# Performance work log

Measured on AMD Instinct MI355X. Metric: run time of the kernel, lower is better.

## Reference

```python
import jax, jax.numpy as jnp
import numpy as np

N = 100000   # nodes
E = 1600000  # edges
D_IN = 128
D_H = 128


def setup_inputs() -> dict:
    key = jax.random.key(0)
    ks = jax.random.split(key, 8)
    s = 1.0 / np.sqrt(D_IN)
    return {
        "x": jax.random.normal(ks[0], (N, D_IN), dtype=jnp.float32),
        "edge_index": jax.random.randint(ks[1], (2, E), 0, N, dtype=jnp.int64),
        "W_l1": jax.random.uniform(ks[2], (D_IN, D_H), jnp.float32, -s, s),
        "b_l1": jnp.zeros((D_H,), jnp.float32),
        "W_r1": jax.random.uniform(ks[3], (D_IN, D_H), jnp.float32, -s, s),
        "W_l2": jax.random.uniform(ks[4], (D_H, D_H), jnp.float32, -s, s),
        "b_l2": jnp.zeros((D_H,), jnp.float32),
        "W_r2": jax.random.uniform(ks[5], (D_H, D_H), jnp.float32, -s, s),
    }


def _sage_layer(z, src, dst, Wl, bl, Wr):
    # message: relu(x_j) gathered along src; aggregate: mean over dst
    msg = jax.nn.relu(z[src])                                   # [E, D]
    summed = jax.ops.segment_sum(msg, dst, num_segments=N)      # [N, D]
    cnt = jax.ops.segment_sum(jnp.ones((src.shape[0],), z.dtype), dst,
                              num_segments=N)                   # [N]
    mean = summed / jnp.maximum(cnt, 1.0)[:, None]
    return mean @ Wl + bl + z @ Wr                              # lin_l + lin_r(root)


def reference(x, edge_index, W_l1, b_l1, W_r1, W_l2, b_l2, W_r2):
    src, dst = edge_index[0], edge_index[1]
    h = _sage_layer(x, src, dst, W_l1, b_l1, W_r1)
    h = jax.nn.relu(h)  # activation between layers; norms are Identity, dropout 0
    return _sage_layer(h, src, dst, W_l2, b_l2, W_r2)
```

## Files before the change

kernel.cpp:

```cpp
#include <hip/hip_runtime.h>

typedef short short8 __attribute__((ext_vector_type(8)));
typedef unsigned short ushort8 __attribute__((ext_vector_type(8)));
typedef float f32x4 __attribute__((ext_vector_type(4)));
typedef float f32x2 __attribute__((ext_vector_type(2)));

__device__ __forceinline__ unsigned short f2bf(float f) {
    unsigned int u = __float_as_uint(f);
    u += 0x7FFFu + ((u >> 16) & 1u);
    return (unsigned short)(u >> 16);
}
__device__ __forceinline__ float bf2f(unsigned short s) {
    return __uint_as_float(((unsigned int)s) << 16);
}


#define BSHIFT 8
#define BCAP   8192
#define EPB    2048
#define STG    4792

__global__ __launch_bounds__(512) void prep_k(const int* __restrict__ ei,
                                              int* __restrict__ bcnt,
                                              unsigned int* __restrict__ bbuf,
                                              int E, int B,
                                              const float* __restrict__ x,
                                              unsigned int* __restrict__ xq,
                                              unsigned int* __restrict__ hqz,
                                              int total4,
                                              const float* __restrict__ W0,
                                              const float* __restrict__ W1,
                                              const float* __restrict__ W2,
                                              const float* __restrict__ W3,
                                              unsigned short* __restrict__ wsz,
                                              int P1B, int CXB) {
    __shared__ int s_cnt[512];
    __shared__ int s_off[512];
    __shared__ int s_wsum[8];
    __shared__ int s_wbase[8];
    __shared__ unsigned int s_gmap[608];
    __shared__ unsigned int stage[STG];
    __shared__ int s_T;
    int tid = threadIdx.x;
    int bx = blockIdx.x;

    if (bx < P1B) {
        s_cnt[tid] = 0;
        __syncthreads();
        int e0 = bx * EPB + tid;
        int dstc[4];
#pragma unroll
        for (int k = 0; k < 4; k++) {
            int e = e0 + k * 512;
            dstc[k] = (e < E) ? ei[E + e] : -1;
            if (e < E) atomicAdd(&s_cnt[dstc[k] >> BSHIFT], 1);
        }
        __syncthreads();
        int c = s_cnt[tid];
        int cpad = (c + 7) & ~7;
        int lane = tid & 63, wid = tid >> 6;
        int incl = cpad;
#pragma unroll
        for (int d = 1; d < 64; d <<= 1) {
            int t = __shfl_up(incl, d);
            if (lane >= d) incl += t;
        }
        if (lane == 63) s_wsum[wid] = incl;
        __syncthreads();
        if (tid < 8) {
            int acc = 0;
            for (int j = 0; j < tid; j++) acc += s_wsum[j];
            s_wbase[tid] = acc;
            if (tid == 7) s_T = acc + s_wsum[7];
        }
        __syncthreads();
        int excl = s_wbase[wid] + incl - cpad;
        int gbase = (c > 0) ? atomicAdd(&bcnt[tid], cpad) : 0;
        unsigned int bb = (unsigned int)tid * BCAP;
        int ng = cpad >> 3;
        for (int k = 0; k < ng; k++) {
            int gw = gbase + (k << 3);
            s_gmap[(excl >> 3) + k] = (gw + 8 <= BCAP) ? (bb + (unsigned int)gw) : 0xFFFFFFFFu;
        }
        for (int j = c; j < cpad; j++) stage[excl + j] = 0xFFFFFFFFu;
        s_off[tid] = excl;
        s_cnt[tid] = 0;
        __syncthreads();
#pragma unroll
        for (int k = 0; k < 4; k++) {
            int e = e0 + k * 512;
            if (e < E) {
                int src = ei[e];
                int dst = dstc[k];
                int b = dst >> BSHIFT;
                int pos = s_off[b] + atomicAdd(&s_cnt[b], 1);
                stage[pos] = ((unsigned int)(dst & 255) << 17) | (unsigned int)src;
            }
        }
        __syncthreads();
        int T = s_T;
        for (int i = tid; i < T; i += 512) {
            unsigned int g = s_gmap[i >> 3];
            if (g != 0xFFFFFFFFu) bbuf[(size_t)g + (i & 7)] = stage[i];
        }
    } else if (bx < P1B + CXB) {
        int base = (bx - P1B) * 2048 + tid;
#pragma unroll
        for (int k = 0; k < 4; k++) {
            int i = base + k * 512;
            if (i < total4) {
                float4 v = ((const float4*)x)[i];
                float rx = fmaxf(v.x, 0.f), ry = fmaxf(v.y, 0.f);
                float rz = fmaxf(v.z, 0.f), rw = fmaxf(v.w, 0.f);
                unsigned int q = (unsigned int)__builtin_amdgcn_cvt_pk_fp8_f32(rx, ry, 0, false);
                q = (unsigned int)__builtin_amdgcn_cvt_pk_fp8_f32(rz, rw, (int)q, true);
                xq[i] = q;
            } else if (i < total4 + 32) {
                xq[i] = 0;
                hqz[i - total4] = 0;
            }
        }
    } else {
        int idx = (bx - P1B - CXB) * 512 + tid;
        if (idx < 4 * 16384) {
            int m = idx >> 14, r = idx & 16383;
            const float* W = (m == 0) ? W0 : (m == 1) ? W1 : (m == 2) ? W2 : W3;
            int k = r >> 7, n = r & 127;
            int t = k >> 5, kg = (k >> 3) & 3, j = k & 7;
            int c = n >> 4, ln = n & 15;
            int dst = (((t * 8 + c) * 64) + kg * 16 + ln) * 8 + j;
            wsz[m * 16384 + dst] = f2bf(W[r]);
        }
    }
}

__global__ __launch_bounds__(512) void p2_k(const unsigned int* __restrict__ bbuf,
                                            const int* __restrict__ bcnt,
                                            int* __restrict__ col,
                                            int* __restrict__ deg, int N) {
    __shared__ int s_deg[256];
    int tid = threadIdx.x;
    int b = blockIdx.x;
    if (tid < 256) s_deg[tid] = 0;
    __syncthreads();
    int cnt = bcnt[b];
    if (cnt > BCAP) cnt = BCAP;
    int nbase = b << BSHIFT;
    for (int i = tid; i < cnt; i += 512) {
        unsigned int p = bbuf[(size_t)b * BCAP + i];
        if (p == 0xFFFFFFFFu) continue;
        int src = (int)(p & 0x1FFFFu);
        int rem = (int)(p >> 17);
        int slot = atomicAdd(&s_deg[rem], 1);
        if (slot < 64) col[(size_t)(nbase + rem) * 64 + slot] = src;
    }
    __syncthreads();
    int n = nbase + tid;
    if (tid < 256 && n < N) {
        int d = s_deg[tid];
        deg[n] = d;
        int dc = min(d, 64);
        int pe = min((dc + 3) & ~3, 64);
        for (int j = dc; j < pe; j++) col[(size_t)n * 64 + j] = N;
    }
}


__global__ __launch_bounds__(256) void agg_q(const unsigned char* __restrict__ hq,
                                             const int* __restrict__ col,
                                             const int* __restrict__ deg,
                                             unsigned short* __restrict__ mean,
                                             int N) {
    int lane = threadIdx.x & 63;
    int g = lane >> 4, l16 = lane & 15;
    int n = (blockIdx.x * 4 + (threadIdx.x >> 6)) * 4 + g;
    if (n >= N) return;
    int m = deg[n];
    if (m > 64) m = 64;
    const int* cp = col + (size_t)n * 64;
    unsigned int lofs = (unsigned int)l16 * 8u;

    f32x2 a[4];
#pragma unroll
    for (int d = 0; d < 4; d++) { a[d].x = 0.f; a[d].y = 0.f; }

    int s0 = cp[0], s1 = cp[1], s2 = cp[2], s3 = cp[3];

#pragma unroll 2
    for (int i = 0; i < m; i += 4) {
        uint2 v0 = *(const uint2*)(hq + ((((unsigned int)s0) << 7) + lofs));
        uint2 v1 = *(const uint2*)(hq + ((((unsigned int)s1) << 7) + lofs));
        uint2 v2 = *(const uint2*)(hq + ((((unsigned int)s2) << 7) + lofs));
        uint2 v3 = *(const uint2*)(hq + ((((unsigned int)s3) << 7) + lofs));
        s0 = cp[i + 4]; s1 = cp[i + 5]; s2 = cp[i + 6]; s3 = cp[i + 7];
#pragma unroll
        for (int k = 0; k < 4; k++) {
            uint2 v = (k == 0) ? v0 : (k == 1) ? v1 : (k == 2) ? v2 : v3;
            f32x2 p0 = __builtin_amdgcn_cvt_pk_f32_fp8((int)v.x, false);
            f32x2 p1 = __builtin_amdgcn_cvt_pk_f32_fp8((int)v.x, true);
            f32x2 p2 = __builtin_amdgcn_cvt_pk_f32_fp8((int)v.y, false);
            f32x2 p3 = __builtin_amdgcn_cvt_pk_f32_fp8((int)v.y, true);
            asm("v_pk_add_f32 %0, %0, %1" : "+v"(a[0]) : "v"(p0));
            asm("v_pk_add_f32 %0, %0, %1" : "+v"(a[1]) : "v"(p1));
            asm("v_pk_add_f32 %0, %0, %1" : "+v"(a[2]) : "v"(p2));
            asm("v_pk_add_f32 %0, %0, %1" : "+v"(a[3]) : "v"(p3));
        }
    }

    float iv = 1.0f / (float)max(m, 1);
    ushort8 p;
#pragma unroll
    for (int d = 0; d < 4; d++) {
        p[2 * d]     = f2bf(a[d].x * iv);
        p[2 * d + 1] = f2bf(a[d].y * iv);
    }
    *(ushort8*)((char*)mean + ((((unsigned int)n) << 8) + (unsigned int)l16 * 16u)) = p;
}


template <bool RELU, bool ZF32, bool OUT_BF16, bool OUT_Q>
__global__ __launch_bounds__(256) void gemm_fused(const unsigned short* __restrict__ A,
                                                  const void* __restrict__ Zv,
                                                  const unsigned short* __restrict__ wsz,
                                                  const float* __restrict__ bias,
                                                  float* __restrict__ outF,
                                                  unsigned short* __restrict__ outB,
                                                  unsigned char* __restrict__ outQ,
                                                  int M, int NG) {
    __shared__ unsigned short smem[32768];
    {
        const int4* src = (const int4*)wsz;
        int4* dst = (int4*)smem;
        for (int i = threadIdx.x; i < 4096; i += 256) dst[i] = src[i];
    }
    __syncthreads();

    int lane = threadIdx.x & 63;
    int wv = threadIdx.x >> 6;
    int r16 = lane & 15, kg = lane >> 4;

    for (int gq = blockIdx.x * 4 + wv; gq < NG; gq += gridDim.x * 4) {
        int rbase = gq * 64;
        short8 af[4][4], zf[4][4];
#pragma unroll
        for (int i = 0; i < 4; i++) {
            int row = rbase + i * 16 + r16;
            if (row < M) {
                const short8* ap = (const short8*)(A + (size_t)row * 128);
#pragma unroll
                for (int t = 0; t < 4; t++) af[i][t] = ap[t * 4 + kg];
                if (ZF32) {
                    const float4* zp = (const float4*)((const float*)Zv + (size_t)row * 128);
#pragma unroll
                    for (int t = 0; t < 4; t++) {
                        float4 a0 = zp[t * 8 + kg * 2];
                        float4 a1 = zp[t * 8 + kg * 2 + 1];
                        short8 z;
                        z[0] = (short)f2bf(a0.x); z[1] = (short)f2bf(a0.y);
                        z[2] = (short)f2bf(a0.z); z[3] = (short)f2bf(a0.w);
                        z[4] = (short)f2bf(a1.x); z[5] = (short)f2bf(a1.y);
                        z[6] = (short)f2bf(a1.z); z[7] = (short)f2bf(a1.w);
                        zf[i][t] = z;
                    }
                } else {
                    const short8* zp = (const short8*)((const unsigned short*)Zv + (size_t)row * 128);
#pragma unroll
                    for (int t = 0; t < 4; t++) zf[i][t] = zp[t * 4 + kg];
                }
            } else {
                short8 zr = {0, 0, 0, 0, 0, 0, 0, 0};
#pragma unroll
                for (int t = 0; t < 4; t++) { af[i][t] = zr; zf[i][t] = zr; }
            }
        }
#pragma unroll
        for (int c = 0; c < 8; c++) {
            float bv = bias[c * 16 + r16];
            f32x4 acc[4];
#pragma unroll
            for (int i = 0; i < 4; i++) acc[i] = (f32x4){bv, bv, bv, bv};
#pragma unroll
            for (int t = 0; t < 4; t++) {
                short8 wa = *(const short8*)(smem + ((t * 8 + c) * 64 + lane) * 8);
#pragma unroll
                for (int i = 0; i < 4; i++)
                    acc[i] = __builtin_amdgcn_mfma_f32_16x16x32_bf16(af[i][t], wa, acc[i], 0, 0, 0);
            }
#pragma unroll
            for (int t = 0; t < 4; t++) {
                short8 wb = *(const short8*)(smem + 16384 + ((t * 8 + c) * 64 + lane) * 8);
#pragma unroll
                for (int i = 0; i < 4; i++)
                    acc[i] = __builtin_amdgcn_mfma_f32_16x16x32_bf16(zf[i][t], wb, acc[i], 0, 0, 0);
            }
#pragma unroll
            for (int i = 0; i < 4; i++) {
#pragma unroll
                for (int r = 0; r < 4; r++) {
                    int orow = rbase + i * 16 + kg * 4 + r;
                    if (orow < M) {
                        float v = acc[i][r];
                        if (RELU) v = fmaxf(v, 0.f);
                        if (OUT_BF16)
                            outB[(size_t)orow * 128 + c * 16 + r16] = f2bf(v);
                        else
                            outF[(size_t)orow * 128 + c * 16 + r16] = v;
                        if (OUT_Q) {
                            unsigned int q = (unsigned int)__builtin_amdgcn_cvt_pk_fp8_f32(v, v, 0, false);
                            outQ[(size_t)orow * 128 + c * 16 + r16] = (unsigned char)(q & 0xFFu);
                        }
                    }
                }
            }
        }
    }
}


extern "C" void kernel_launch(void* const* d_in, const int* in_sizes, int n_in,
                              void* d_out, int out_size, void* d_ws, size_t ws_size,
                              hipStream_t stream) {
    const float* x   = (const float*)d_in[0];
    const int*   ei  = (const int*)d_in[1];
    const float* Wl1 = (const float*)d_in[2];
    const float* bl1 = (const float*)d_in[3];
    const float* Wr1 = (const float*)d_in[4];
    const float* Wl2 = (const float*)d_in[5];
    const float* bl2 = (const float*)d_in[6];
    const float* Wr2 = (const float*)d_in[7];

    int N = in_sizes[0] / 128;
    int E = in_sizes[1] / 2;
    int B = (N + 255) >> BSHIFT;

    char* ws = (char*)d_ws;
    size_t off = 0;
    auto alloc = [&](size_t bytes) -> char* {
        char* p = ws + off;
        off += (bytes + 255) & ~(size_t)255;
        return p;
    };
    int*   deg  = (int*)alloc((size_t)N * 4);
    int*   bcnt = (int*)alloc((size_t)B * 4);
    unsigned short* meanB = (unsigned short*)alloc((size_t)N * 128 * 2);
    unsigned short* hb    = (unsigned short*)alloc((size_t)(N + 1) * 128 * 2);
    unsigned short* wsz   = (unsigned short*)alloc(4 * 16384 * 2);

    unsigned int* bbuf = (unsigned int*)meanB;
    unsigned char* xq  = (unsigned char*)hb;
    int* col = (int*)d_out;
    unsigned char* hq = (unsigned char*)d_out + (size_t)N * 64 * 4;

    hipMemsetAsync(bcnt, 0, (size_t)B * 4, stream);

    int total4 = N * 32;
    int P1B = (E + EPB - 1) / EPB;
    int CXB = (total4 + 32 + 2047) / 2048;
    int CWB = (4 * 16384 + 511) / 512;
    prep_k<<<P1B + CXB + CWB, 512, 0, stream>>>(
        ei, bcnt, bbuf, E, B,
        x, (unsigned int*)xq, (unsigned int*)(hq + (size_t)N * 128), total4,
        Wl1, Wr1, Wl2, Wr2, wsz, P1B, CXB);
    p2_k<<<B, 512, 0, stream>>>(bbuf, bcnt, col, deg, N);

    int NT = (N + 15) / 16;
    int NG = (NT + 3) / 4;
    int GB = (NG + 3) / 4;
    agg_q<<<(N + 15) / 16, 256, 0, stream>>>(xq, col, deg, meanB, N);
    gemm_fused<true, true, true, true><<<GB, 256, 0, stream>>>(meanB, x, wsz, bl1,
                                                               nullptr, hb, hq, N, NG);
    agg_q<<<(N + 15) / 16, 256, 0, stream>>>(hq, col, deg, meanB, N);
    gemm_fused<false, false, false, false><<<GB, 256, 0, stream>>>(meanB, hb, wsz + 32768, bl2,
                                                                   (float*)d_out, nullptr, nullptr, N, NG);
}
```

Before: 271.8 us.

## Fuse neighbor mean aggregation into the MFMA GEMM kernels

Removes the separate agg_q kernels and performs the fp8 neighbor gather and mean inside each GEMM wave, building the bf16 A fragments directly in registers. This drops the bf16 mean buffer's write and read-back and two kernel launches. Workspace is reorganized: the col list moves out of d_out, the hidden bf16 layer is stored in d_out with a 512-byte row stride, and the second layer overwrites it in place. In exchange, each row's gather is spread over only 4 lanes with strided 8-byte loads, register pressure rises, and the GEMM grid is small. The gather may therefore become latency-bound with little parallelism to hide it.

```diff
diff --git a/kernel.cpp b/kernel.cpp
--- a/kernel.cpp
+++ b/kernel.cpp
@@ -10,8 +10,16 @@
     u += 0x7FFFu + ((u >> 16) & 1u);
     return (unsigned short)(u >> 16);
 }
-__device__ __forceinline__ float bf2f(unsigned short s) {
-    return __uint_as_float(((unsigned int)s) << 16);
+
+__device__ __forceinline__ void acc8(f32x2* a, uint2 v) {
+    f32x2 p0 = __builtin_amdgcn_cvt_pk_f32_fp8((int)v.x, false);
+    f32x2 p1 = __builtin_amdgcn_cvt_pk_f32_fp8((int)v.x, true);
+    f32x2 p2 = __builtin_amdgcn_cvt_pk_f32_fp8((int)v.y, false);
+    f32x2 p3 = __builtin_amdgcn_cvt_pk_f32_fp8((int)v.y, true);
+    asm("v_pk_add_f32 %0, %0, %1" : "+v"(a[0]) : "v"(p0));
+    asm("v_pk_add_f32 %0, %0, %1" : "+v"(a[1]) : "v"(p1));
+    asm("v_pk_add_f32 %0, %0, %1" : "+v"(a[2]) : "v"(p2));
+    asm("v_pk_add_f32 %0, %0, %1" : "+v"(a[3]) : "v"(p3));
 }
 
 
@@ -26,7 +34,6 @@
                                               int E, int B,
                                               const float* __restrict__ x,
                                               unsigned int* __restrict__ xq,
-                                              unsigned int* __restrict__ hqz,
                                               int total4,
                                               const float* __restrict__ W0,
                                               const float* __restrict__ W1,
@@ -117,7 +124,6 @@
                 xq[i] = q;
             } else if (i < total4 + 32) {
                 xq[i] = 0;
-                hqz[i - total4] = 0;
             }
         }
     } else {
@@ -166,73 +172,24 @@
 }
 
 
-__global__ __launch_bounds__(256) void agg_q(const unsigned char* __restrict__ hq,
-                                             const int* __restrict__ col,
-                                             const int* __restrict__ deg,
-                                             unsigned short* __restrict__ mean,
-                                             int N) {
-    int lane = threadIdx.x & 63;
-    int g = lane >> 4, l16 = lane & 15;
-    int n = (blockIdx.x * 4 + (threadIdx.x >> 6)) * 4 + g;
-    if (n >= N) return;
-    int m = deg[n];
-    if (m > 64) m = 64;
-    const int* cp = col + (size_t)n * 64;
-    unsigned int lofs = (unsigned int)l16 * 8u;
-
-    f32x2 a[4];
-#pragma unroll
-    for (int d = 0; d < 4; d++) { a[d].x = 0.f; a[d].y = 0.f; }
-
-    int s0 = cp[0], s1 = cp[1], s2 = cp[2], s3 = cp[3];
-
-#pragma unroll 2
-    for (int i = 0; i < m; i += 4) {
-        uint2 v0 = *(const uint2*)(hq + ((((unsigned int)s0) << 7) + lofs));
-        uint2 v1 = *(const uint2*)(hq + ((((unsigned int)s1) << 7) + lofs));
-        uint2 v2 = *(const uint2*)(hq + ((((unsigned int)s2) << 7) + lofs));
-        uint2 v3 = *(const uint2*)(hq + ((((unsigned int)s3) << 7) + lofs));
-        s0 = cp[i + 4]; s1 = cp[i + 5]; s2 = cp[i + 6]; s3 = cp[i + 7];
-#pragma unroll
-        for (int k = 0; k < 4; k++) {
-            uint2 v = (k == 0) ? v0 : (k == 1) ? v1 : (k == 2) ? v2 : v3;
-            f32x2 p0 = __builtin_amdgcn_cvt_pk_f32_fp8((int)v.x, false);
-            f32x2 p1 = __builtin_amdgcn_cvt_pk_f32_fp8((int)v.x, true);
-            f32x2 p2 = __builtin_amdgcn_cvt_pk_f32_fp8((int)v.y, false);
-            f32x2 p3 = __builtin_amdgcn_cvt_pk_f32_fp8((int)v.y, true);
-            asm("v_pk_add_f32 %0, %0, %1" : "+v"(a[0]) : "v"(p0));
-            asm("v_pk_add_f32 %0, %0, %1" : "+v"(a[1]) : "v"(p1));
-            asm("v_pk_add_f32 %0, %0, %1" : "+v"(a[2]) : "v"(p2));
-            asm("v_pk_add_f32 %0, %0, %1" : "+v"(a[3]) : "v"(p3));
-        }
-    }
-
-    float iv = 1.0f / (float)max(m, 1);
-    ushort8 p;
-#pragma unroll
-    for (int d = 0; d < 4; d++) {
-        p[2 * d]     = f2bf(a[d].x * iv);
-        p[2 * d + 1] = f2bf(a[d].y * iv);
-    }
-    *(ushort8*)((char*)mean + ((((unsigned int)n) << 8) + (unsigned int)l16 * 16u)) = p;
-}
-
-
-template <bool RELU, bool ZF32, bool OUT_BF16, bool OUT_Q>
-__global__ __launch_bounds__(256) void gemm_fused(const unsigned short* __restrict__ A,
-                                                  const void* __restrict__ Zv,
-                                                  const unsigned short* __restrict__ wsz,
-                                                  const float* __restrict__ bias,
-                                                  float* __restrict__ outF,
-                                                  unsigned short* __restrict__ outB,
-                                                  unsigned char* __restrict__ outQ,
-                                                  int M, int NG) {
+template <bool L1>
+__global__ __launch_bounds__(256) void gemm_gather(const unsigned char* __restrict__ tab,
+                                                   const int* __restrict__ col,
+                                                   const int* __restrict__ deg,
+                                                   const void* __restrict__ Zv,
+                                                   const unsigned short* __restrict__ wsz,
+                                                   const float* __restrict__ bias,
+                                                   void* __restrict__ outp,
+                                                   unsigned char* __restrict__ outQ,
+                                                   int M, int NG) {
     __shared__ unsigned short smem[32768];
     {
         const int4* src = (const int4*)wsz;
         int4* dst = (int4*)smem;
         for (int i = threadIdx.x; i < 4096; i += 256) dst[i] = src[i];
     }
+    if (L1 && blockIdx.x == 0 && threadIdx.x < 32)
+        ((unsigned int*)(outQ + (size_t)M * 128))[threadIdx.x] = 0;
     __syncthreads();
 
     int lane = threadIdx.x & 63;
@@ -242,14 +199,55 @@
     for (int gq = blockIdx.x * 4 + wv; gq < NG; gq += gridDim.x * 4) {
         int rbase = gq * 64;
         short8 af[4][4], zf[4][4];
+
+#pragma unroll
+        for (int i = 0; i < 4; i++) {
+            int row = rbase + i * 16 + r16;
+            f32x2 a[16];
+#pragma unroll
+            for (int q = 0; q < 16; q++) { a[q].x = 0.f; a[q].y = 0.f; }
+            int m = 0;
+            if (row < M) {
+                m = deg[row];
+                if (m > 64) m = 64;
+                const int* cp = col + (size_t)row * 64;
+                const unsigned char* tb = tab + kg * 8;
+#pragma unroll 2
+                for (int it = 0; it < m; it += 4) {
+                    int myidx = cp[it + kg];
+#pragma unroll
+                    for (int k = 0; k < 4; k++) {
+                        int s = __shfl(myidx, r16 + k * 16);
+                        const unsigned char* rp = tb + ((size_t)(unsigned int)s << 7);
+                        uint2 v0 = *(const uint2*)(rp);
+                        uint2 v1 = *(const uint2*)(rp + 32);
+                        uint2 v2 = *(const uint2*)(rp + 64);
+                        uint2 v3 = *(const uint2*)(rp + 96);
+                        acc8(&a[0], v0);
+                        acc8(&a[4], v1);
+                        acc8(&a[8], v2);
+                        acc8(&a[12], v3);
+                    }
+                }
+            }
+            float iv = 1.0f / (float)max(m, 1);
+#pragma unroll
+            for (int t = 0; t < 4; t++) {
+                short8 z;
+#pragma unroll
+                for (int j = 0; j < 4; j++) {
+                    z[2 * j]     = (short)f2bf(a[t * 4 + j].x * iv);
+                    z[2 * j + 1] = (short)f2bf(a[t * 4 + j].y * iv);
+                }
+                af[i][t] = z;
+            }
+        }
+
 #pragma unroll
         for (int i = 0; i < 4; i++) {
             int row = rbase + i * 16 + r16;
             if (row < M) {
-                const short8* ap = (const short8*)(A + (size_t)row * 128);
-#pragma unroll
-                for (int t = 0; t < 4; t++) af[i][t] = ap[t * 4 + kg];
-                if (ZF32) {
+                if (L1) {
                     const float4* zp = (const float4*)((const float*)Zv + (size_t)row * 128);
 #pragma unroll
                     for (int t = 0; t < 4; t++) {
@@ -263,16 +261,17 @@
                         zf[i][t] = z;
                     }
                 } else {
-                    const short8* zp = (const short8*)((const unsigned short*)Zv + (size_t)row * 128);
+                    const short8* zp = (const short8*)((const char*)Zv + (size_t)row * 512);
 #pragma unroll
                     for (int t = 0; t < 4; t++) zf[i][t] = zp[t * 4 + kg];
                 }
             } else {
                 short8 zr = {0, 0, 0, 0, 0, 0, 0, 0};
 #pragma unroll
-                for (int t = 0; t < 4; t++) { af[i][t] = zr; zf[i][t] = zr; }
-            }
-        }
+                for (int t = 0; t < 4; t++) zf[i][t] = zr;
+            }
+        }
+
 #pragma unroll
         for (int c = 0; c < 8; c++) {
             float bv = bias[c * 16 + r16];
@@ -300,14 +299,13 @@
                     int orow = rbase + i * 16 + kg * 4 + r;
                     if (orow < M) {
                         float v = acc[i][r];
-                        if (RELU) v = fmaxf(v, 0.f);
-                        if (OUT_BF16)
-                            outB[(size_t)orow * 128 + c * 16 + r16] = f2bf(v);
-                        else
-                            outF[(size_t)orow * 128 + c * 16 + r16] = v;
-                        if (OUT_Q) {
-                            unsigned int q = (unsigned int)__builtin_amdgcn_cvt_pk_fp8_f32(v, v, 0, false);
+                        if (L1) {
+                            float rv = fmaxf(v, 0.f);
+                            ((unsigned short*)outp)[(size_t)orow * 256 + c * 16 + r16] = f2bf(rv);
+                            unsigned int q = (unsigned int)__builtin_amdgcn_cvt_pk_fp8_f32(rv, rv, 0, false);
                             outQ[(size_t)orow * 128 + c * 16 + r16] = (unsigned char)(q & 0xFFu);
+                        } else {
+                            ((float*)outp)[(size_t)orow * 128 + c * 16 + r16] = v;
                         }
                     }
                 }
@@ -340,16 +338,15 @@
         off += (bytes + 255) & ~(size_t)255;
         return p;
     };
-    int*   deg  = (int*)alloc((size_t)N * 4);
-    int*   bcnt = (int*)alloc((size_t)B * 4);
-    unsigned short* meanB = (unsigned short*)alloc((size_t)N * 128 * 2);
-    unsigned short* hb    = (unsigned short*)alloc((size_t)(N + 1) * 128 * 2);
-    unsigned short* wsz   = (unsigned short*)alloc(4 * 16384 * 2);
-
-    unsigned int* bbuf = (unsigned int*)meanB;
-    unsigned char* xq  = (unsigned char*)hb;
-    int* col = (int*)d_out;
-    unsigned char* hq = (unsigned char*)d_out + (size_t)N * 64 * 4;
+    int* deg  = (int*)alloc((size_t)N * 4);
+    int* bcnt = (int*)alloc((size_t)B * 4);
+    int* col  = (int*)alloc((size_t)N * 64 * 4);
+    unsigned char* xq = (unsigned char*)alloc((size_t)(N + 1) * 128);
+    unsigned char* hqbb = (unsigned char*)alloc((size_t)B * BCAP * 4);
+    unsigned short* wsz = (unsigned short*)alloc(4 * 16384 * 2);
+
+    unsigned int* bbuf = (unsigned int*)hqbb;
+    unsigned char* hq  = hqbb;
 
     hipMemsetAsync(bcnt, 0, (size_t)B * 4, stream);
 
@@ -358,18 +355,15 @@
     int CXB = (total4 + 32 + 2047) / 2048;
     int CWB = (4 * 16384 + 511) / 512;
     prep_k<<<P1B + CXB + CWB, 512, 0, stream>>>(
-        ei, bcnt, bbuf, E, B,
-        x, (unsigned int*)xq, (unsigned int*)(hq + (size_t)N * 128), total4,
+        ei, bcnt, bbuf, E, B, x, (unsigned int*)xq, total4,
         Wl1, Wr1, Wl2, Wr2, wsz, P1B, CXB);
     p2_k<<<B, 512, 0, stream>>>(bbuf, bcnt, col, deg, N);
 
     int NT = (N + 15) / 16;
     int NG = (NT + 3) / 4;
     int GB = (NG + 3) / 4;
-    agg_q<<<(N + 15) / 16, 256, 0, stream>>>(xq, col, deg, meanB, N);
-    gemm_fused<true, true, true, true><<<GB, 256, 0, stream>>>(meanB, x, wsz, bl1,
-                                                               nullptr, hb, hq, N, NG);
-    agg_q<<<(N + 15) / 16, 256, 0, stream>>>(hq, col, deg, meanB, N);
-    gemm_fused<false, false, false, false><<<GB, 256, 0, stream>>>(meanB, hb, wsz + 32768, bl2,
-                                                                   (float*)d_out, nullptr, nullptr, N, NG);
-}
+    gemm_gather<true><<<GB, 256, 0, stream>>>(xq, col, deg, x, wsz, bl1,
+                                              d_out, hq, N, NG);
+    gemm_gather<false><<<GB, 256, 0, stream>>>(hq, col, deg, d_out, wsz + 32768, bl2,
+                                               d_out, nullptr, N, NG);
+}
```

Measured after the change: 387.3 us. 42.5% more time.
